# Kernel optimization log

Hardware: AMD Instinct MI355X
Metric: run time of the kernel (lower is better)

## Reference

```python
import jax, jax.numpy as jnp
import numpy as np

DIM = 1024
NUM_HEADS = 16
HEAD_DIM = DIM // NUM_HEADS
EPS = 1e-5


def setup_inputs() -> dict:
    key = jax.random.key(0)
    ks = jax.random.split(key, 5)
    B, N = 2, 2048
    x = jax.random.normal(ks[0], (B, N, DIM), dtype=jnp.float32)
    # nn.Linear(dim, 3*dim): weight [3*dim, dim], bias [3*dim]
    w_qkv = jax.random.normal(ks[1], (3 * DIM, DIM), dtype=jnp.float32) * (DIM ** -0.5)
    b_qkv = jnp.zeros((3 * DIM,), dtype=jnp.float32)
    # qk-norm LayerNorm(head_dim) affine params
    q_gamma = jnp.ones((HEAD_DIM,), dtype=jnp.float32)
    q_beta = jnp.zeros((HEAD_DIM,), dtype=jnp.float32)
    k_gamma = jnp.ones((HEAD_DIM,), dtype=jnp.float32)
    k_beta = jnp.zeros((HEAD_DIM,), dtype=jnp.float32)
    # output projection nn.Linear(dim, dim)
    w_proj = jax.random.normal(ks[2], (DIM, DIM), dtype=jnp.float32) * (DIM ** -0.5)
    b_proj = jnp.zeros((DIM,), dtype=jnp.float32)
    return {
        "x": x,
        "w_qkv": w_qkv, "b_qkv": b_qkv,
        "q_gamma": q_gamma, "q_beta": q_beta,
        "k_gamma": k_gamma, "k_beta": k_beta,
        "w_proj": w_proj, "b_proj": b_proj,
    }


def _layernorm(t, gamma, beta):
    # LayerNorm over last dim (head_dim)
    mu = jnp.mean(t, axis=-1, keepdims=True)
    var = jnp.mean(jnp.square(t - mu), axis=-1, keepdims=True)
    return (t - mu) * jax.lax.rsqrt(var + EPS) * gamma + beta


def reference(x, w_qkv, b_qkv, q_gamma, q_beta, k_gamma, k_beta, w_proj, b_proj):
    B, N, C = x.shape
    H, D = NUM_HEADS, HEAD_DIM
    scale = D ** -0.5
    # QKV projection: [B,N,3C] -> [3,B,H,N,D]
    qkv = x @ w_qkv.T + b_qkv
    qkv = qkv.reshape(B, N, 3, H, D).transpose(2, 0, 3, 1, 4)
    q, k, v = qkv[0], qkv[1], qkv[2]
    # per-head qk-norm
    q = _layernorm(q, q_gamma, q_beta)
    k = _layernorm(k, k_gamma, k_beta)
    # scaled dot-product attention
    scores = jnp.einsum("bhqd,bhkd->bhqk", q, k) * scale
    attn = jax.nn.softmax(scores, axis=-1)
    out = jnp.einsum("bhqk,bhkd->bhqd", attn, v)  # [B,H,N,D]
    out = out.transpose(0, 2, 1, 3).reshape(B, N, C)
    # output projection
    return out @ w_proj.T + b_proj
```

## Files before the change

kernel.cpp:

```cpp
#include <hip/hip_runtime.h>

typedef _Float16 half8 __attribute__((ext_vector_type(8)));
typedef _Float16 half4 __attribute__((ext_vector_type(4)));
typedef float f32x4 __attribute__((ext_vector_type(4)));
typedef float f32x16 __attribute__((ext_vector_type(16)));
typedef unsigned int uint;
typedef uint uint2v __attribute__((ext_vector_type(2)));
typedef uint uint4v __attribute__((ext_vector_type(4)));

#define MFMA16(a, b, c) __builtin_amdgcn_mfma_f32_16x16x32_f16((a), (b), (c), 0, 0, 0)
#define MFMA32(a, b, c) __builtin_amdgcn_mfma_f32_32x32x16_f16((a), (b), (c), 0, 0, 0)

#define GLOAD16(g, l)                                            \
    __builtin_amdgcn_global_load_lds(                            \
        (const __attribute__((address_space(1))) void*)(g),      \
        (__attribute__((address_space(3))) void*)(l), 16, 0, 0)


__global__ __launch_bounds__(256) void cvt_all(const float* __restrict__ x,
                                               const float* __restrict__ wq,
                                               const float* __restrict__ wp,
                                               _Float16* __restrict__ xh,
                                               _Float16* __restrict__ wqh,
                                               _Float16* __restrict__ wph) {
    int i = blockIdx.x * 256 + threadIdx.x;
    const float* src;
    _Float16* dst;
    int off;
    if (i < 524288) { src = x; dst = xh; off = i; }
    else if (i < 917504) { src = wq; dst = wqh; off = i - 524288; }
    else { src = wp; dst = wph; off = i - 917504; }
    const float4* p = reinterpret_cast<const float4*>(src) + 2 * (size_t)off;
    float4 a = p[0], b = p[1];
    half8 o;
    o[0] = (_Float16)a.x; o[1] = (_Float16)a.y; o[2] = (_Float16)a.z; o[3] = (_Float16)a.w;
    o[4] = (_Float16)b.x; o[5] = (_Float16)b.y; o[6] = (_Float16)b.z; o[7] = (_Float16)b.w;
    reinterpret_cast<half8*>(dst)[off] = o;
}

template <int MT, int NT, int EPI>
__global__ __launch_bounds__(256) void gemm_nt(const _Float16* __restrict__ A,
                                               const _Float16* __restrict__ W,
                                               const float* __restrict__ bias,
                                               void* __restrict__ Cout, int K,
                                               const float* __restrict__ qg,
                                               const float* __restrict__ qb,
                                               const float* __restrict__ kg,
                                               const float* __restrict__ kb) {
    constexpr int TM = MT * 32;
    constexpr int TN = NT * 32;
    __shared__ __align__(16) _Float16 Al[2][TM * 64];
    __shared__ __align__(16) _Float16 Wl[2][TN * 64];
    const int tid = threadIdx.x, l = tid & 63, w = tid >> 6;
    const int lin = blockIdx.x + (blockIdx.y << 6);
    const int nwg = gridDim.x * gridDim.y;
    const int wg = (lin & 7) * (nwg >> 3) + (lin >> 3);
    const int bm = (wg & 63) * TM, bn = (wg >> 6) * TN;
    const int wr = (w >> 1) * (MT * 16), wc = (w & 1) * (NT * 16);
    const int srow = l >> 3;
    const int schunk = (l & 7) ^ srow;

    const _Float16* Ag = A + (size_t)(bm + (TM / 4) * w + srow) * K + 8 * schunk;
    const _Float16* Wg = W + (size_t)(bn + (TN / 4) * w + srow) * K + 8 * schunk;
    const int rswz = (l & 7) << 3;
    const int nk = K >> 6;

    auto stage = [&](int t, int buf) {
        const int kt = t << 6;
#pragma unroll
        for (int i = 0; i < MT; i++)
            GLOAD16(Ag + (size_t)(8 * i) * K + kt, &Al[buf][((TM / 4) * w + 8 * i) * 64]);
#pragma unroll
        for (int i = 0; i < NT; i++)
            GLOAD16(Wg + (size_t)(8 * i) * K + kt, &Wl[buf][((TN / 4) * w + 8 * i) * 64]);
    };

    f32x4 acc[MT][NT] = {};
    stage(0, 0);
    __syncthreads();
    for (int t = 0; t < nk; ++t) {
        const int cur = t & 1;
        if (t + 1 < nk) stage(t + 1, cur ^ 1);
#pragma unroll
        for (int ks = 0; ks < 2; ks++) {
            const int koff = (ks * 32 + (l >> 4) * 8) ^ rswz;
            half8 af[MT], wf[NT];
#pragma unroll
            for (int i = 0; i < MT; i++)
                af[i] = *(const half8*)&Al[cur][(wr + i * 16 + (l & 15)) * 64 + koff];
#pragma unroll
            for (int i = 0; i < NT; i++)
                wf[i] = *(const half8*)&Wl[cur][(wc + i * 16 + (l & 15)) * 64 + koff];
            __builtin_amdgcn_s_setprio(1);
#pragma unroll
            for (int mt = 0; mt < MT; mt++)
#pragma unroll
                for (int nt = 0; nt < NT; nt++)
                    acc[mt][nt] = MFMA16(af[mt], wf[nt], acc[mt][nt]);
            __builtin_amdgcn_s_setprio(0);
        }
        __syncthreads();
    }

    if (EPI == 0) {
        const int ncol = bn + wc;
        const int s = ncol >> 10;
        const int hh = (ncol >> 6) & 15;
        const float* gam = (s == 0) ? qg : kg;
        const float* bet = (s == 0) ? qb : kb;
        float ga[4], be[4];
        if (s < 2) {
#pragma unroll
            for (int nt = 0; nt < 4; nt++) {
                int d = nt * 16 + (l & 15);
                ga[nt] = gam[d];
                be[nt] = bet[d];
            }
        }
        const float cs = (s == 0) ? 0.18033688f : 1.f;
#pragma unroll
        for (int mt = 0; mt < MT; mt++)
#pragma unroll
            for (int r = 0; r < 4; r++) {
                float v[4];
                float sm = 0.f, s2 = 0.f;
#pragma unroll
                for (int nt = 0; nt < 4; nt++) {
                    v[nt] = acc[mt][nt][r] + bias[ncol + nt * 16 + (l & 15)];
                    sm += v[nt];
                    s2 += v[nt] * v[nt];
                }
                int m = bm + wr + mt * 16 + (l >> 4) * 4 + r;
                int b = m >> 11, nn = m & 2047;
                _Float16* dst = (_Float16*)Cout +
                    (size_t)((((s * 2 + b) * 16 + hh) * 2048 + nn) << 6);
                if (s < 2) {
#pragma unroll
                    for (int off = 1; off < 16; off <<= 1) {
                        sm += __shfl_xor(sm, off);
                        s2 += __shfl_xor(s2, off);
                    }
                    float mean = sm * (1.f / 64.f);
                    float var = s2 * (1.f / 64.f) - mean * mean;
                    float rs = rsqrtf(var + 1e-5f) * cs;
#pragma unroll
                    for (int nt = 0; nt < 4; nt++) {
                        int d = nt * 16 + (l & 15);
                        dst[d] = (_Float16)((v[nt] - mean) * rs * ga[nt] + be[nt] * cs);
                    }
                } else {
#pragma unroll
                    for (int nt = 0; nt < 4; nt++)
                        dst[nt * 16 + (l & 15)] = (_Float16)v[nt];
                }
            }
    } else {
#pragma unroll
        for (int mt = 0; mt < MT; mt++)
#pragma unroll
            for (int nt = 0; nt < NT; nt++)
#pragma unroll
                for (int r = 0; r < 4; r++) {
                    int m = bm + wr + mt * 16 + (l >> 4) * 4 + r;
                    int n = bn + wc + nt * 16 + (l & 15);
                    ((float*)Cout)[(size_t)m * 1024 + n] = acc[mt][nt][r] + bias[n];
                }
    }
}

template <int SPLIT>
__global__ __launch_bounds__(256, 4) void attn_kernel(const _Float16* __restrict__ qkv,
                                                      _Float16* __restrict__ out,
                                                      float* __restrict__ lpart) {
    const int tid = threadIdx.x;
    const int l = tid & 63, w = tid >> 6;
    const int l31 = l & 31, hi = l >> 5;
    const int bid = blockIdx.x;
    const int nwg = 512 * SPLIT;
    const int wg = (bid & 7) * (nwg >> 3) + (bid >> 3);
    int head, qt, quarter;
    if (SPLIT == 4) { head = wg >> 6; qt = (wg >> 2) & 15; quarter = wg & 3; }
    else            { head = wg >> 4; qt = wg & 15;        quarter = 0; }
    const int b = head >> 4, h = head & 15;
    const size_t hstride = (size_t)2048 * 64;
    const _Float16* Q = qkv + (size_t)((0 + b) * 16 + h) * hstride;
    const _Float16* Kp = qkv + (size_t)((2 + b) * 16 + h) * hstride + (size_t)quarter * 512 * 64;
    const _Float16* Vp = qkv + (size_t)((4 + b) * 16 + h) * hstride + (size_t)quarter * 512 * 64;
    const int NIT = (SPLIT == 4) ? 8 : 32;

    __shared__ __align__(16) _Float16 Kl[2][64 * 64];
    __shared__ __align__(16) _Float16 Vt[2][64 * 64];

    const int r0q = qt * 128 + w * 32;
    half8 qf[4];
    {
        const _Float16* Qrow = Q + (size_t)(r0q + l31) * 64 + 8 * hi;
#pragma unroll
        for (int dk = 0; dk < 4; dk++) qf[dk] = *(const half8*)&Qrow[16 * dk];
    }

    const int srow = l >> 3, sch = l & 7;
    auto stageK = [&](int it, _Float16* dst) {
#pragma unroll
        for (int t = 0; t < 2; t++) {
            int r0 = 16 * w + 8 * t;
            const _Float16* g = Kp + (size_t)(it * 64 + r0 + srow) * 64 + 8 * (sch ^ srow);
            GLOAD16(g, &dst[r0 * 64]);
        }
    };
    auto loadV = [&](int it, half8& v0, half8& v1) {
        const _Float16* g = Vp + (size_t)(it * 64 + 16 * w + srow) * 64 + 8 * sch;
        v0 = *(const half8*)g;
        v1 = *(const half8*)(g + 8 * 64);
    };
    auto scatterV = [&](half8 v0, half8 v1, _Float16* dst) {
        const int j0 = 16 * w + srow;
        const int d0 = 8 * sch;
#pragma unroll
        for (int i = 0; i < 8; i++) {
            const int sw = (i ^ sch) << 3;
            dst[(d0 + i) * 64 + (j0 ^ sw)] = v0[i];
            dst[(d0 + i) * 64 + ((j0 + 8) ^ sw)] = v1[i];
        }
    };

    float lrun = 0.f;
    f32x16 o0 = {}, o1 = {};

    half8 va, vb;
    stageK(0, Kl[0]);
    loadV(0, va, vb);
    scatterV(va, vb, Vt[0]);
    __syncthreads();

    const int kswz = (l31 & 7) << 3;
    const int vswz0 = ((l31 & 7) ^ (l31 >> 3)) << 3;
    const int vswz1 = vswz0 ^ (4 << 3);

    for (int it = 0; it < NIT; ++it) {
        const int cur = it & 1;
        const _Float16* Kc = Kl[cur];
        const _Float16* Vc = Vt[cur];
        if (it + 1 < NIT) {
            stageK(it + 1, Kl[cur ^ 1]);
            loadV(it + 1, va, vb);
        }

#pragma unroll
        for (int hf = 0; hf < 2; hf++) {
            f32x16 st = {};
#pragma unroll
            for (int dk = 0; dk < 4; dk++) {
                const int colr = 16 * dk + 8 * hi;
                half8 kf = *(const half8*)&Kc[(hf * 32 + l31) * 64 + (colr ^ kswz)];
                __builtin_amdgcn_s_setprio(1);
                st = MFMA32(kf, qf[dk], st);
                __builtin_amdgcn_s_setprio(0);
            }
#pragma unroll
            for (int r = 0; r < 16; r++) st[r] = exp2f(st[r]);
            lrun += (((st[0] + st[1]) + (st[2] + st[3])) +
                     ((st[4] + st[5]) + (st[6] + st[7]))) +
                    (((st[8] + st[9]) + (st[10] + st[11])) +
                     ((st[12] + st[13]) + (st[14] + st[15])));

#pragma unroll
            for (int cc = 0; cc < 2; cc++) {
                const int c = 2 * hf + cc;
                uint pk0 = __builtin_bit_cast(uint, __builtin_amdgcn_cvt_pkrtz(st[cc * 8 + 0], st[cc * 8 + 1]));
                uint pk1 = __builtin_bit_cast(uint, __builtin_amdgcn_cvt_pkrtz(st[cc * 8 + 2], st[cc * 8 + 3]));
                uint pk2 = __builtin_bit_cast(uint, __builtin_amdgcn_cvt_pkrtz(st[cc * 8 + 4], st[cc * 8 + 5]));
                uint pk3 = __builtin_bit_cast(uint, __builtin_amdgcn_cvt_pkrtz(st[cc * 8 + 6], st[cc * 8 + 7]));
                uint2v s02 = __builtin_amdgcn_permlane32_swap(pk0, pk2, false, false);
                uint2v s13 = __builtin_amdgcn_permlane32_swap(pk1, pk3, false, false);
                uint4v fu = {s02.x, s13.x, s02.y, s13.y};
                half8 pfrag = __builtin_bit_cast(half8, fu);
                const int colc = 16 * c + 8 * hi;
                half8 vf0 = *(const half8*)&Vc[l31 * 64 + (colc ^ vswz0)];
                half8 vf1 = *(const half8*)&Vc[(32 + l31) * 64 + (colc ^ vswz1)];
                __builtin_amdgcn_s_setprio(1);
                o0 = MFMA32(vf0, pfrag, o0);
                o1 = MFMA32(vf1, pfrag, o1);
                __builtin_amdgcn_s_setprio(0);
            }
        }

        if (it + 1 < NIT) scatterV(va, vb, Vt[cur ^ 1]);
        __syncthreads();
    }

    lrun += __shfl_xor(lrun, 32);
    const int tok = r0q + l31;
    if (SPLIT == 4) {
        _Float16* orow = out + (size_t)quarter * 4194304 + (size_t)(b * 2048 + tok) * 1024 + h * 64;
#pragma unroll
        for (int g = 0; g < 4; g++) {
            half4 h4a, h4b;
#pragma unroll
            for (int j = 0; j < 4; j++) {
                h4a[j] = (_Float16)o0[4 * g + j];
                h4b[j] = (_Float16)o1[4 * g + j];
            }
            *(half4*)&orow[8 * g + 4 * hi] = h4a;
            *(half4*)&orow[32 + 8 * g + 4 * hi] = h4b;
        }
        if (!hi) lpart[quarter * 65536 + (b * 16 + h) * 2048 + tok] = lrun;
    } else {
        const float inv = __builtin_amdgcn_rcpf(lrun);
        _Float16* orow = out + (size_t)(b * 2048 + tok) * 1024 + h * 64;
#pragma unroll
        for (int g = 0; g < 4; g++) {
            half4 h4a, h4b;
#pragma unroll
            for (int j = 0; j < 4; j++) {
                h4a[j] = (_Float16)(o0[4 * g + j] * inv);
                h4b[j] = (_Float16)(o1[4 * g + j] * inv);
            }
            *(half4*)&orow[8 * g + 4 * hi] = h4a;
            *(half4*)&orow[32 + 8 * g + 4 * hi] = h4b;
        }
    }
}

__global__ __launch_bounds__(256) void merge_attn(const _Float16* __restrict__ onum,
                                                  const float* __restrict__ lpart,
                                                  _Float16* __restrict__ attnh) {
    const int i = blockIdx.x * 256 + threadIdx.x;
    const int tokb = i >> 7;
    const int c0 = (i & 127) * 8;
    const int h = c0 >> 6;
    const int bb = tokb >> 11, tok = tokb & 2047;
    const int li = (bb * 16 + h) * 2048 + tok;
    float lt = lpart[li] + lpart[65536 + li] + lpart[131072 + li] + lpart[196608 + li];
    float inv = __builtin_amdgcn_rcpf(lt);
    float acc[8] = {};
#pragma unroll
    for (int q = 0; q < 4; q++) {
        half8 v = *(const half8*)&onum[(size_t)q * 4194304 + (size_t)tokb * 1024 + c0];
#pragma unroll
        for (int j = 0; j < 8; j++) acc[j] += (float)v[j];
    }
    half8 o;
#pragma unroll
    for (int j = 0; j < 8; j++) o[j] = (_Float16)(acc[j] * inv);
    *(half8*)&attnh[(size_t)tokb * 1024 + c0] = o;
}

extern "C" void kernel_launch(void* const* d_in, const int* in_sizes, int n_in,
                              void* d_out, int out_size, void* d_ws, size_t ws_size,
                              hipStream_t stream) {
    const float* x = (const float*)d_in[0];
    const float* w_qkv = (const float*)d_in[1];
    const float* b_qkv = (const float*)d_in[2];
    const float* q_gamma = (const float*)d_in[3];
    const float* q_beta = (const float*)d_in[4];
    const float* k_gamma = (const float*)d_in[5];
    const float* k_beta = (const float*)d_in[6];
    const float* w_proj = (const float*)d_in[7];
    const float* b_proj = (const float*)d_in[8];

    char* ws = (char*)d_ws;
    _Float16* xh = (_Float16*)(ws + 0);
    _Float16* wqkvh = (_Float16*)(ws + 8388608);
    _Float16* wprojh = (_Float16*)(ws + 14680064);
    _Float16* qkvh = (_Float16*)(ws + 16777216);
    _Float16* attnh = (_Float16*)(ws + 41943040);
    _Float16* onum = (_Float16*)(ws + 50331648);
    float* lp = (float*)(ws + 83886080);
    const bool split = ws_size >= 84934656;

    cvt_all<<<4096, 256, 0, stream>>>(x, w_qkv, w_proj, xh, wqkvh, wprojh);

    gemm_nt<2, 4, 0><<<dim3(64, 24), 256, 0, stream>>>(xh, wqkvh, b_qkv, (void*)qkvh, 1024,
                                                       q_gamma, q_beta, k_gamma, k_beta);

    if (split) {
        attn_kernel<4><<<2048, 256, 0, stream>>>(qkvh, onum, lp);
        merge_attn<<<2048, 256, 0, stream>>>(onum, lp, attnh);
    } else {
        attn_kernel<1><<<512, 256, 0, stream>>>(qkvh, attnh, nullptr);
    }

    gemm_nt<2, 2, 1><<<dim3(64, 16), 256, 0, stream>>>(attnh, wprojh, b_proj, d_out, 1024,
                                                       nullptr, nullptr, nullptr, nullptr);
}
```

Measured before the change: 224.8 us.

## Retile GEMMs, single-buffer GEMM LDS, XCD-aware block mapping, split-KV attention by two

The GEMM kernel drops double buffering in favour of a single LDS buffer with two barriers per k-step, and gains a new XCD-aware block-to-tile mapping parameterised by template arguments. The QKV GEMM moves to 128x128 tiles and the projection GEMM to 64x128 tiles. Attention now splits the KV sequence into two parts instead of four, with a two-way merge kernel, and V loads are issued after compute instead of being prefetched into registers. The goal is more reuse per tile, better L2 locality and less merge traffic, at the cost of losing load/compute overlap in the GEMM and exposing V load latency.

Result: faster. 208.5 us (-7.3%).

```diff
diff --git a/kernel.cpp b/kernel.cpp
--- a/kernel.cpp
+++ b/kernel.cpp
@@ -38,7 +38,7 @@
     reinterpret_cast<half8*>(dst)[off] = o;
 }
 
-template <int MT, int NT, int EPI>
+template <int MT, int NT, int EPI, int RIML2, int RIN>
 __global__ __launch_bounds__(256) void gemm_nt(const _Float16* __restrict__ A,
                                                const _Float16* __restrict__ W,
                                                const float* __restrict__ bias,
@@ -49,48 +49,44 @@
                                                const float* __restrict__ kb) {
     constexpr int TM = MT * 32;
     constexpr int TN = NT * 32;
-    __shared__ __align__(16) _Float16 Al[2][TM * 64];
-    __shared__ __align__(16) _Float16 Wl[2][TN * 64];
+    __shared__ __align__(16) _Float16 Al[TM * 64];
+    __shared__ __align__(16) _Float16 Wl[TN * 64];
     const int tid = threadIdx.x, l = tid & 63, w = tid >> 6;
-    const int lin = blockIdx.x + (blockIdx.y << 6);
-    const int nwg = gridDim.x * gridDim.y;
-    const int wg = (lin & 7) * (nwg >> 3) + (lin >> 3);
-    const int bm = (wg & 63) * TM, bn = (wg >> 6) * TN;
+    const int lin = blockIdx.x + blockIdx.y * gridDim.x;
+    const int xcd = lin & 7, idx = lin >> 3;
+    const int im = idx & ((1 << RIML2) - 1), in = idx >> RIML2;
+    const int bm = ((xcd & 3) * (1 << RIML2) + im) * TM;
+    const int bn = ((xcd >> 2) * RIN + in) * TN;
     const int wr = (w >> 1) * (MT * 16), wc = (w & 1) * (NT * 16);
     const int srow = l >> 3;
     const int schunk = (l & 7) ^ srow;
+    const int rswz = (l & 7) << 3;
 
     const _Float16* Ag = A + (size_t)(bm + (TM / 4) * w + srow) * K + 8 * schunk;
     const _Float16* Wg = W + (size_t)(bn + (TN / 4) * w + srow) * K + 8 * schunk;
-    const int rswz = (l & 7) << 3;
     const int nk = K >> 6;
 
-    auto stage = [&](int t, int buf) {
+    f32x4 acc[MT][NT] = {};
+    for (int t = 0; t < nk; ++t) {
         const int kt = t << 6;
+        __syncthreads();
 #pragma unroll
         for (int i = 0; i < MT; i++)
-            GLOAD16(Ag + (size_t)(8 * i) * K + kt, &Al[buf][((TM / 4) * w + 8 * i) * 64]);
+            GLOAD16(Ag + (size_t)(8 * i) * K + kt, &Al[((TM / 4) * w + 8 * i) * 64]);
 #pragma unroll
         for (int i = 0; i < NT; i++)
-            GLOAD16(Wg + (size_t)(8 * i) * K + kt, &Wl[buf][((TN / 4) * w + 8 * i) * 64]);
-    };
-
-    f32x4 acc[MT][NT] = {};
-    stage(0, 0);
-    __syncthreads();
-    for (int t = 0; t < nk; ++t) {
-        const int cur = t & 1;
-        if (t + 1 < nk) stage(t + 1, cur ^ 1);
+            GLOAD16(Wg + (size_t)(8 * i) * K + kt, &Wl[((TN / 4) * w + 8 * i) * 64]);
+        __syncthreads();
 #pragma unroll
         for (int ks = 0; ks < 2; ks++) {
             const int koff = (ks * 32 + (l >> 4) * 8) ^ rswz;
             half8 af[MT], wf[NT];
 #pragma unroll
             for (int i = 0; i < MT; i++)
-                af[i] = *(const half8*)&Al[cur][(wr + i * 16 + (l & 15)) * 64 + koff];
+                af[i] = *(const half8*)&Al[(wr + i * 16 + (l & 15)) * 64 + koff];
 #pragma unroll
             for (int i = 0; i < NT; i++)
-                wf[i] = *(const half8*)&Wl[cur][(wc + i * 16 + (l & 15)) * 64 + koff];
+                wf[i] = *(const half8*)&Wl[(wc + i * 16 + (l & 15)) * 64 + koff];
             __builtin_amdgcn_s_setprio(1);
 #pragma unroll
             for (int mt = 0; mt < MT; mt++)
@@ -99,7 +95,6 @@
                     acc[mt][nt] = MFMA16(af[mt], wf[nt], acc[mt][nt]);
             __builtin_amdgcn_s_setprio(0);
         }
-        __syncthreads();
     }
 
     if (EPI == 0) {
@@ -172,21 +167,23 @@
 __global__ __launch_bounds__(256, 4) void attn_kernel(const _Float16* __restrict__ qkv,
                                                       _Float16* __restrict__ out,
                                                       float* __restrict__ lpart) {
+    constexpr int LS = (SPLIT == 4) ? 2 : (SPLIT == 2) ? 1 : 0;
     const int tid = threadIdx.x;
     const int l = tid & 63, w = tid >> 6;
     const int l31 = l & 31, hi = l >> 5;
     const int bid = blockIdx.x;
     const int nwg = 512 * SPLIT;
     const int wg = (bid & 7) * (nwg >> 3) + (bid >> 3);
-    int head, qt, quarter;
-    if (SPLIT == 4) { head = wg >> 6; qt = (wg >> 2) & 15; quarter = wg & 3; }
-    else            { head = wg >> 4; qt = wg & 15;        quarter = 0; }
+    const int part = wg & (SPLIT - 1);
+    const int qt = (wg >> LS) & 15;
+    const int head = wg >> (4 + LS);
     const int b = head >> 4, h = head & 15;
     const size_t hstride = (size_t)2048 * 64;
+    const int kvlen = 2048 / SPLIT;
     const _Float16* Q = qkv + (size_t)((0 + b) * 16 + h) * hstride;
-    const _Float16* Kp = qkv + (size_t)((2 + b) * 16 + h) * hstride + (size_t)quarter * 512 * 64;
-    const _Float16* Vp = qkv + (size_t)((4 + b) * 16 + h) * hstride + (size_t)quarter * 512 * 64;
-    const int NIT = (SPLIT == 4) ? 8 : 32;
+    const _Float16* Kp = qkv + (size_t)((2 + b) * 16 + h) * hstride + (size_t)part * kvlen * 64;
+    const _Float16* Vp = qkv + (size_t)((4 + b) * 16 + h) * hstride + (size_t)part * kvlen * 64;
+    const int NIT = kvlen / 64;
 
     __shared__ __align__(16) _Float16 Kl[2][64 * 64];
     __shared__ __align__(16) _Float16 Vt[2][64 * 64];
@@ -208,12 +205,10 @@
             GLOAD16(g, &dst[r0 * 64]);
         }
     };
-    auto loadV = [&](int it, half8& v0, half8& v1) {
+    auto loadScatterV = [&](int it, _Float16* dst) {
         const _Float16* g = Vp + (size_t)(it * 64 + 16 * w + srow) * 64 + 8 * sch;
-        v0 = *(const half8*)g;
-        v1 = *(const half8*)(g + 8 * 64);
-    };
-    auto scatterV = [&](half8 v0, half8 v1, _Float16* dst) {
+        half8 v0 = *(const half8*)g;
+        half8 v1 = *(const half8*)(g + 8 * 64);
         const int j0 = 16 * w + srow;
         const int d0 = 8 * sch;
 #pragma unroll
@@ -227,10 +222,8 @@
     float lrun = 0.f;
     f32x16 o0 = {}, o1 = {};
 
-    half8 va, vb;
     stageK(0, Kl[0]);
-    loadV(0, va, vb);
-    scatterV(va, vb, Vt[0]);
+    loadScatterV(0, Vt[0]);
     __syncthreads();
 
     const int kswz = (l31 & 7) << 3;
@@ -241,10 +234,7 @@
         const int cur = it & 1;
         const _Float16* Kc = Kl[cur];
         const _Float16* Vc = Vt[cur];
-        if (it + 1 < NIT) {
-            stageK(it + 1, Kl[cur ^ 1]);
-            loadV(it + 1, va, vb);
-        }
+        if (it + 1 < NIT) stageK(it + 1, Kl[cur ^ 1]);
 
 #pragma unroll
         for (int hf = 0; hf < 2; hf++) {
@@ -285,14 +275,14 @@
             }
         }
 
-        if (it + 1 < NIT) scatterV(va, vb, Vt[cur ^ 1]);
+        if (it + 1 < NIT) loadScatterV(it + 1, Vt[cur ^ 1]);
         __syncthreads();
     }
 
     lrun += __shfl_xor(lrun, 32);
     const int tok = r0q + l31;
-    if (SPLIT == 4) {
-        _Float16* orow = out + (size_t)quarter * 4194304 + (size_t)(b * 2048 + tok) * 1024 + h * 64;
+    if (SPLIT > 1) {
+        _Float16* orow = out + (size_t)part * 4194304 + (size_t)(b * 2048 + tok) * 1024 + h * 64;
 #pragma unroll
         for (int g = 0; g < 4; g++) {
             half4 h4a, h4b;
@@ -304,7 +294,7 @@
             *(half4*)&orow[8 * g + 4 * hi] = h4a;
             *(half4*)&orow[32 + 8 * g + 4 * hi] = h4b;
         }
-        if (!hi) lpart[quarter * 65536 + (b * 16 + h) * 2048 + tok] = lrun;
+        if (!hi) lpart[part * 65536 + (b * 16 + h) * 2048 + tok] = lrun;
     } else {
         const float inv = __builtin_amdgcn_rcpf(lrun);
         _Float16* orow = out + (size_t)(b * 2048 + tok) * 1024 + h * 64;
@@ -322,20 +312,20 @@
     }
 }
 
-__global__ __launch_bounds__(256) void merge_attn(const _Float16* __restrict__ onum,
-                                                  const float* __restrict__ lpart,
-                                                  _Float16* __restrict__ attnh) {
+__global__ __launch_bounds__(256) void merge_attn2(const _Float16* __restrict__ onum,
+                                                   const float* __restrict__ lpart,
+                                                   _Float16* __restrict__ attnh) {
     const int i = blockIdx.x * 256 + threadIdx.x;
     const int tokb = i >> 7;
     const int c0 = (i & 127) * 8;
     const int h = c0 >> 6;
     const int bb = tokb >> 11, tok = tokb & 2047;
     const int li = (bb * 16 + h) * 2048 + tok;
-    float lt = lpart[li] + lpart[65536 + li] + lpart[131072 + li] + lpart[196608 + li];
+    float lt = lpart[li] + lpart[65536 + li];
     float inv = __builtin_amdgcn_rcpf(lt);
     float acc[8] = {};
 #pragma unroll
-    for (int q = 0; q < 4; q++) {
+    for (int q = 0; q < 2; q++) {
         half8 v = *(const half8*)&onum[(size_t)q * 4194304 + (size_t)tokb * 1024 + c0];
 #pragma unroll
         for (int j = 0; j < 8; j++) acc[j] += (float)v[j];
@@ -366,21 +356,21 @@
     _Float16* qkvh = (_Float16*)(ws + 16777216);
     _Float16* attnh = (_Float16*)(ws + 41943040);
     _Float16* onum = (_Float16*)(ws + 50331648);
-    float* lp = (float*)(ws + 83886080);
-    const bool split = ws_size >= 84934656;
+    float* lp = (float*)(ws + 67108864);
+    const bool split = ws_size >= 67633152;
 
     cvt_all<<<4096, 256, 0, stream>>>(x, w_qkv, w_proj, xh, wqkvh, wprojh);
 
-    gemm_nt<2, 4, 0><<<dim3(64, 24), 256, 0, stream>>>(xh, wqkvh, b_qkv, (void*)qkvh, 1024,
-                                                       q_gamma, q_beta, k_gamma, k_beta);
+    gemm_nt<4, 4, 0, 3, 12><<<dim3(32, 24), 256, 0, stream>>>(
+        xh, wqkvh, b_qkv, (void*)qkvh, 1024, q_gamma, q_beta, k_gamma, k_beta);
 
     if (split) {
-        attn_kernel<4><<<2048, 256, 0, stream>>>(qkvh, onum, lp);
-        merge_attn<<<2048, 256, 0, stream>>>(onum, lp, attnh);
+        attn_kernel<2><<<1024, 256, 0, stream>>>(qkvh, onum, lp);
+        merge_attn2<<<2048, 256, 0, stream>>>(onum, lp, attnh);
     } else {
         attn_kernel<1><<<512, 256, 0, stream>>>(qkvh, attnh, nullptr);
     }
 
-    gemm_nt<2, 2, 1><<<dim3(64, 16), 256, 0, stream>>>(attnh, wprojh, b_proj, d_out, 1024,
-                                                       nullptr, nullptr, nullptr, nullptr);
-}
+    gemm_nt<2, 4, 1, 4, 4><<<dim3(64, 8), 256, 0, stream>>>(
+        attnh, wprojh, b_proj, d_out, 1024, nullptr, nullptr, nullptr, nullptr);
+}
```
